# Performance work log

Hardware: AMD Instinct MI355X
Metric: run time of the kernel (lower is better)

The kernel has to match this reference:

```python
import jax, jax.numpy as jnp
import numpy as np
from jax import lax

IN_CH = 32
OUT_CH = 32
K = 7
PAD = 3
STRIDE = 1


def setup_inputs() -> dict:
    key = jax.random.key(0)
    k1, k2, k3 = jax.random.split(key, 3)
    B, T = 4, 4096
    x = jax.random.normal(k1, (B, IN_CH, T), dtype=jnp.float32)
    # weight-generating conv params: [out*in*k, in, k]
    fan_in = IN_CH * K
    W = jax.random.normal(k2, (OUT_CH * IN_CH * K, IN_CH, K), dtype=jnp.float32) / np.sqrt(fan_in).astype(np.float32)
    b = jax.random.normal(k3, (OUT_CH * IN_CH * K,), dtype=jnp.float32) * 0.01
    return {"x": x, "W": W, "b": b}


def _unfold1d(x):
    # x: [B, C, L]; pad then stack K shifted views -> [B, C, K, T]
    xp = jnp.pad(x, ((0, 0), (0, 0), (PAD, PAD)))
    Lp = xp.shape[-1]
    T = Lp - K + 1
    return jnp.stack([xp[:, :, i:i + T:STRIDE] for i in range(K)], axis=2)


def reference(x, W, b):
    B, C, L = x.shape
    # dynamic weight generation: conv1d, same padding -> [B, out*in*K, T]
    dw = lax.conv_general_dilated(
        x, W, window_strides=(STRIDE,), padding=[(PAD, PAD)],
        dimension_numbers=("NCH", "OIH", "NCH"))
    dw = dw + b[None, :, None]
    dw = dw.reshape(B, OUT_CH, IN_CH, K, -1)  # [B, O, I, K, T]
    dw = jax.nn.softmax(dw / np.sqrt(K).astype(np.float32), axis=3)
    x_unf = _unfold1d(x)  # [B, I, K, T]
    y = jnp.einsum("bckt,bockt->bot", x_unf, dw)
    return y
```

## Files before the change

kernel.cpp:

```cpp
#include <hip/hip_runtime.h>
#include <hip/hip_bf16.h>


typedef unsigned short u16;
typedef unsigned int u32;
typedef __attribute__((ext_vector_type(8))) short short8;
typedef __attribute__((ext_vector_type(4))) float f32x4;

#define IN_CH 32
#define OUT_CH 32
#define KW 7
#define TSZ 4096
#define BSZ 4
#define CONTR 224
#define NROWS 7168
#define BLK_T 512
#define XS_STRIDE 40
#define XS_ROWS (BLK_T + 6)
#define SLICE_U16 3584
#define CH_U16 25088
#define CEXP2 0.54528747f

__device__ __forceinline__ u32 f2bf(float v) {
    u32 b = __float_as_uint(v);
    return (b + 0x7fffu + ((b >> 16) & 1u)) >> 16;
}

__device__ __forceinline__ void glds16(const u16* g, u16* l) {
    __builtin_amdgcn_global_load_lds((__attribute__((address_space(1))) void*)g,
                                     (__attribute__((address_space(3))) void*)l,
                                     16, 0, 0);
}

__global__ __launch_bounds__(512)
void wprep(const float* __restrict__ W, const float* __restrict__ bias,
           u16* __restrict__ Wp, float* __restrict__ bp) {
    __shared__ float ws[CH_U16];
    int ch  = blockIdx.x;
    int tid = threadIdx.x;
    const float* src = W + (size_t)ch * CH_U16;
    #pragma unroll
    for (int it = 0; it < 49; ++it)
        ws[it * 512 + tid] = src[it * 512 + tid];
    __syncthreads();
    u16* dst = Wp + (size_t)ch * CH_U16;
    #pragma unroll
    for (int it = 0; it < 49; ++it) {
        int oidx = it * 512 + tid;
        int e  = oidx & 7;
        int pp = (oidx >> 3) & 3;
        int t1 = oidx >> 5;
        int rp = t1 % 112;
        int j  = t1 / 112;
        int p  = pp ^ ((rp >> 1) & 3);
        int c  = p * 8 + e;
        int k  = rp >> 4;
        int q  = rp & 15;
        dst[oidx] = (u16)f2bf(ws[(q * 7 + k) * CONTR + c * 7 + j]);
    }
    if (tid < 112) {
        int k = tid >> 4, q = tid & 15;
        int gp = ch * 16 + q;
        int o = gp >> 5, i = gp & 31;
        bp[ch * 112 + tid] = bias[(o * IN_CH + i) * KW + k];
    }
}

__global__ __launch_bounds__(256)
void xprep(const float* __restrict__ x, u16* __restrict__ xT) {
    int bid = blockIdx.x;
    int b = bid >> 6;
    int t0 = (bid & 63) * 64;
    __shared__ float lds[32][65];
    int tid = threadIdx.x;
    #pragma unroll
    for (int it = 0; it < 8; ++it) {
        int gi = it * 256 + tid;
        int c = gi >> 6;
        int t = gi & 63;
        lds[c][t] = x[((size_t)b * IN_CH + c) * TSZ + t0 + t];
    }
    __syncthreads();
    #pragma unroll
    for (int it = 0; it < 4; ++it) {
        int wi = it * 256 + tid;
        int t  = wi >> 4;
        int cp = wi & 15;
        u32 b0 = f2bf(lds[cp * 2][t]);
        u32 b1 = f2bf(lds[cp * 2 + 1][t]);
        ((u32*)xT)[((size_t)b * TSZ + t0 + t) * 16 + cp] = b0 | (b1 << 16);
    }
}

__global__ __launch_bounds__(512, 1)
void dconv_main(const u16* __restrict__ Wp, const float* __restrict__ bp,
                const u16* __restrict__ xT, float* __restrict__ out) {
    __shared__ u16 xs[XS_ROWS * XS_STRIDE];
    __shared__ u16 wbuf[2][CH_U16];

    int tid  = threadIdx.x;
    int lane = tid & 63;
    int wave = tid >> 6;
    int g    = lane >> 4;
    int col  = lane & 15;

    int bid = blockIdx.x;
    int b   = bid & 3;
    int tt  = (bid >> 2) & 7;
    int os  = bid >> 5;
    int t0  = tt * BLK_T;

    #pragma unroll
    for (int it = 0; it < 17; ++it) {
        int wi = it * 512 + tid;
        if (wi < XS_ROWS * 16) {
            int row = wi >> 4;
            int cp  = wi & 15;
            int t = t0 - 3 + row;
            u32 v = 0;
            if (t >= 0 && t < TSZ)
                v = ((const u32*)xT)[((size_t)b * TSZ + t) * 16 + cp];
            *(u32*)&xs[row * XS_STRIDE + cp * 2] = v;
        }
    }

    if (wave < 7) {
        const u16* src = Wp + (size_t)(os * 8) * CH_U16 + wave * SLICE_U16 + lane * 8;
        u16* dst = &wbuf[0][wave * SLICE_U16];
        #pragma unroll
        for (int it = 0; it < 7; ++it) glds16(src + it * 512, dst + it * 512);
    }
    __syncthreads();

    int laneA = col * 32 + ((g ^ ((col >> 1) & 3)) * 8);
    int colw0 = wave * 64 + col;

    float yacc[4] = {0.f, 0.f, 0.f, 0.f};

    #pragma unroll 1
    for (int ci = 0; ci < 8; ++ci) {
        int cur = ci & 1;
        if (ci < 7 && wave < 7) {
            const u16* src = Wp + (size_t)(os * 8 + ci + 1) * CH_U16 + wave * SLICE_U16 + lane * 8;
            u16* dst = &wbuf[cur ^ 1][wave * SLICE_U16];
            #pragma unroll
            for (int it = 0; it < 7; ++it) glds16(src + it * 512, dst + it * 512);
        }

        int ch = os * 8 + ci;
        int cc = ci & 1;

        f32x4 acc[7][4];
        const float* bsrc = bp + ch * 112 + g * 4;
        #pragma unroll
        for (int m = 0; m < 7; ++m) {
            f32x4 bv = *(const f32x4*)(bsrc + m * 16);
            acc[m][0] = bv; acc[m][1] = bv; acc[m][2] = bv; acc[m][3] = bv;
        }

        const u16* wl = &wbuf[cur][laneA];
        #pragma unroll
        for (int j = 0; j < 7; ++j) {
            short8 bf[4];
            #pragma unroll
            for (int ct = 0; ct < 4; ++ct)
                bf[ct] = *(const short8*)&xs[(colw0 + ct * 16 + j) * XS_STRIDE + g * 8];
            #pragma unroll
            for (int m = 0; m < 7; ++m) {
                short8 af = *(const short8*)(wl + j * SLICE_U16 + m * 512);
                acc[m][0] = __builtin_amdgcn_mfma_f32_16x16x32_bf16(af, bf[0], acc[m][0], 0, 0, 0);
                acc[m][1] = __builtin_amdgcn_mfma_f32_16x16x32_bf16(af, bf[1], acc[m][1], 0, 0, 0);
                acc[m][2] = __builtin_amdgcn_mfma_f32_16x16x32_bf16(af, bf[2], acc[m][2], 0, 0, 0);
                acc[m][3] = __builtin_amdgcn_mfma_f32_16x16x32_bf16(af, bf[3], acc[m][3], 0, 0, 0);
            }
        }

        __syncthreads();

        int ibase = cc * 16 + g * 4;
        #pragma unroll
        for (int ct = 0; ct < 4; ++ct) {
            int colw = colw0 + ct * 16;
            u32 xv0[7], xv1[7];
            #pragma unroll
            for (int k = 0; k < 7; ++k) {
                const u32* px = (const u32*)&xs[(colw + k) * XS_STRIDE + ibase];
                xv0[k] = px[0]; xv1[k] = px[1];
            }
            #pragma unroll
            for (int r = 0; r < 4; ++r) {
                float ssum = 0.f, psum = 0.f;
                #pragma unroll
                for (int k = 0; k < 7; ++k) {
                    float e = __builtin_amdgcn_exp2f(acc[k][ct][r] * CEXP2);
                    u32 w = (r & 2) ? xv1[k] : xv0[k];
                    float xf = __uint_as_float((r & 1) ? (w & 0xffff0000u) : (w << 16));
                    ssum += e;
                    psum = fmaf(e, xf, psum);
                }
                yacc[ct] += psum * __builtin_amdgcn_rcpf(ssum);
            }
        }

        if (cc == 1) {
            int o = os * 4 + (ci >> 1);
            #pragma unroll
            for (int ct = 0; ct < 4; ++ct) {
                float v = yacc[ct];
                v += __shfl_xor(v, 16, 64);
                v += __shfl_xor(v, 32, 64);
                if (lane < 16)
                    out[((size_t)b * OUT_CH + o) * TSZ + t0 + wave * 64 + ct * 16 + col] = v;
                yacc[ct] = 0.f;
            }
        }
    }
}

extern "C" void kernel_launch(void* const* d_in, const int* in_sizes, int n_in,
                              void* d_out, int out_size, void* d_ws, size_t ws_size,
                              hipStream_t stream) {
    const float* x    = (const float*)d_in[0];
    const float* W    = (const float*)d_in[1];
    const float* bias = (const float*)d_in[2];
    float* out = (float*)d_out;

    u16*   Wp = (u16*)d_ws;
    float* bp = (float*)((char*)d_ws + 3211264);
    u16*   xT = (u16*)((char*)d_ws + 3211264 + 28672);

    hipLaunchKernelGGL(wprep, dim3(64), dim3(512), 0, stream, W, bias, Wp, bp);
    hipLaunchKernelGGL(xprep, dim3(BSZ * (TSZ / 64)), dim3(256), 0, stream, x, xT);
    hipLaunchKernelGGL(dconv_main, dim3(256), dim3(512), 0, stream, Wp, bp, xT, out);
}
```

Before: 124.4 us.

## Halve time tile, single weight buffer split-half prefetch, fold softmax scale into weights

```diff
diff --git a/kernel.cpp b/kernel.cpp
--- a/kernel.cpp
+++ b/kernel.cpp
@@ -14,11 +14,14 @@
 #define BSZ 4
 #define CONTR 224
 #define NROWS 7168
-#define BLK_T 512
-#define XS_STRIDE 40
+#define BLK_T 256
+#define XS_STRIDE 42
 #define XS_ROWS (BLK_T + 6)
 #define SLICE_U16 3584
 #define CH_U16 25088
+#define HALF0_U16 14336
+#define HALF0_UNITS 28
+#define HALF1_UNITS 21
 #define CEXP2 0.54528747f
 
 __device__ __forceinline__ u32 f2bf(float v) {
@@ -56,13 +59,13 @@
         int c  = p * 8 + e;
         int k  = rp >> 4;
         int q  = rp & 15;
-        dst[oidx] = (u16)f2bf(ws[(q * 7 + k) * CONTR + c * 7 + j]);
+        dst[oidx] = (u16)f2bf(ws[(q * 7 + k) * CONTR + c * 7 + j] * CEXP2);
     }
     if (tid < 112) {
         int k = tid >> 4, q = tid & 15;
         int gp = ch * 16 + q;
         int o = gp >> 5, i = gp & 31;
-        bp[ch * 112 + tid] = bias[(o * IN_CH + i) * KW + k];
+        bp[ch * 112 + tid] = bias[(o * IN_CH + i) * KW + k] * CEXP2;
     }
 }
 
@@ -92,11 +95,11 @@
     }
 }
 
-__global__ __launch_bounds__(512, 1)
+__global__ __launch_bounds__(256, 2)
 void dconv_main(const u16* __restrict__ Wp, const float* __restrict__ bp,
                 const u16* __restrict__ xT, float* __restrict__ out) {
     __shared__ u16 xs[XS_ROWS * XS_STRIDE];
-    __shared__ u16 wbuf[2][CH_U16];
+    __shared__ u16 wbuf[CH_U16];
 
     int tid  = threadIdx.x;
     int lane = tid & 63;
@@ -106,13 +109,13 @@
 
     int bid = blockIdx.x;
     int b   = bid & 3;
-    int tt  = (bid >> 2) & 7;
-    int os  = bid >> 5;
+    int tt  = (bid >> 2) & 15;
+    int os  = bid >> 6;
     int t0  = tt * BLK_T;
 
     #pragma unroll
     for (int it = 0; it < 17; ++it) {
-        int wi = it * 512 + tid;
+        int wi = it * 256 + tid;
         if (wi < XS_ROWS * 16) {
             int row = wi >> 4;
             int cp  = wi & 15;
@@ -124,11 +127,10 @@
         }
     }
 
-    if (wave < 7) {
-        const u16* src = Wp + (size_t)(os * 8) * CH_U16 + wave * SLICE_U16 + lane * 8;
-        u16* dst = &wbuf[0][wave * SLICE_U16];
-        #pragma unroll
-        for (int it = 0; it < 7; ++it) glds16(src + it * 512, dst + it * 512);
+    {
+        const u16* src = Wp + (size_t)(os * 8) * CH_U16 + lane * 8;
+        for (int u = wave; u < HALF0_UNITS; u += 4)
+            glds16(src + u * 512, &wbuf[u * 512]);
     }
     __syncthreads();
 
@@ -139,16 +141,14 @@
 
     #pragma unroll 1
     for (int ci = 0; ci < 8; ++ci) {
-        int cur = ci & 1;
-        if (ci < 7 && wave < 7) {
-            const u16* src = Wp + (size_t)(os * 8 + ci + 1) * CH_U16 + wave * SLICE_U16 + lane * 8;
-            u16* dst = &wbuf[cur ^ 1][wave * SLICE_U16];
-            #pragma unroll
-            for (int it = 0; it < 7; ++it) glds16(src + it * 512, dst + it * 512);
-        }
-
         int ch = os * 8 + ci;
         int cc = ci & 1;
+
+        {
+            const u16* src = Wp + (size_t)ch * CH_U16 + 4 * SLICE_U16 + lane * 8;
+            for (int u = wave; u < HALF1_UNITS; u += 4)
+                glds16(src + u * 512, &wbuf[HALF0_U16 + u * 512]);
+        }
 
         f32x4 acc[7][4];
         const float* bsrc = bp + ch * 112 + g * 4;
@@ -158,24 +158,55 @@
             acc[m][0] = bv; acc[m][1] = bv; acc[m][2] = bv; acc[m][3] = bv;
         }
 
-        const u16* wl = &wbuf[cur][laneA];
-        #pragma unroll
-        for (int j = 0; j < 7; ++j) {
-            short8 bf[4];
-            #pragma unroll
-            for (int ct = 0; ct < 4; ++ct)
-                bf[ct] = *(const short8*)&xs[(colw0 + ct * 16 + j) * XS_STRIDE + g * 8];
-            #pragma unroll
-            for (int m = 0; m < 7; ++m) {
-                short8 af = *(const short8*)(wl + j * SLICE_U16 + m * 512);
-                acc[m][0] = __builtin_amdgcn_mfma_f32_16x16x32_bf16(af, bf[0], acc[m][0], 0, 0, 0);
-                acc[m][1] = __builtin_amdgcn_mfma_f32_16x16x32_bf16(af, bf[1], acc[m][1], 0, 0, 0);
-                acc[m][2] = __builtin_amdgcn_mfma_f32_16x16x32_bf16(af, bf[2], acc[m][2], 0, 0, 0);
-                acc[m][3] = __builtin_amdgcn_mfma_f32_16x16x32_bf16(af, bf[3], acc[m][3], 0, 0, 0);
-            }
-        }
-
+        __builtin_amdgcn_s_setprio(1);
+        {
+            const u16* wl = &wbuf[laneA];
+            #pragma unroll
+            for (int j = 0; j < 4; ++j) {
+                short8 bf[4];
+                #pragma unroll
+                for (int ct = 0; ct < 4; ++ct)
+                    bf[ct] = *(const short8*)&xs[(colw0 + ct * 16 + j) * XS_STRIDE + g * 8];
+                #pragma unroll
+                for (int m = 0; m < 7; ++m) {
+                    short8 af = *(const short8*)(wl + j * SLICE_U16 + m * 512);
+                    acc[m][0] = __builtin_amdgcn_mfma_f32_16x16x32_bf16(af, bf[0], acc[m][0], 0, 0, 0);
+                    acc[m][1] = __builtin_amdgcn_mfma_f32_16x16x32_bf16(af, bf[1], acc[m][1], 0, 0, 0);
+                    acc[m][2] = __builtin_amdgcn_mfma_f32_16x16x32_bf16(af, bf[2], acc[m][2], 0, 0, 0);
+                    acc[m][3] = __builtin_amdgcn_mfma_f32_16x16x32_bf16(af, bf[3], acc[m][3], 0, 0, 0);
+                }
+            }
+        }
+        __builtin_amdgcn_s_setprio(0);
         __syncthreads();
+
+        if (ci < 7) {
+            const u16* src = Wp + (size_t)(ch + 1) * CH_U16 + lane * 8;
+            for (int u = wave; u < HALF0_UNITS; u += 4)
+                glds16(src + u * 512, &wbuf[u * 512]);
+        }
+
+        __builtin_amdgcn_s_setprio(1);
+        {
+            const u16* wl = &wbuf[HALF0_U16 + laneA];
+            #pragma unroll
+            for (int jj = 0; jj < 3; ++jj) {
+                int j = 4 + jj;
+                short8 bf[4];
+                #pragma unroll
+                for (int ct = 0; ct < 4; ++ct)
+                    bf[ct] = *(const short8*)&xs[(colw0 + ct * 16 + j) * XS_STRIDE + g * 8];
+                #pragma unroll
+                for (int m = 0; m < 7; ++m) {
+                    short8 af = *(const short8*)(wl + jj * SLICE_U16 + m * 512);
+                    acc[m][0] = __builtin_amdgcn_mfma_f32_16x16x32_bf16(af, bf[0], acc[m][0], 0, 0, 0);
+                    acc[m][1] = __builtin_amdgcn_mfma_f32_16x16x32_bf16(af, bf[1], acc[m][1], 0, 0, 0);
+                    acc[m][2] = __builtin_amdgcn_mfma_f32_16x16x32_bf16(af, bf[2], acc[m][2], 0, 0, 0);
+                    acc[m][3] = __builtin_amdgcn_mfma_f32_16x16x32_bf16(af, bf[3], acc[m][3], 0, 0, 0);
+                }
+            }
+        }
+        __builtin_amdgcn_s_setprio(0);
 
         int ibase = cc * 16 + g * 4;
         #pragma unroll
@@ -192,7 +223,7 @@
                 float ssum = 0.f, psum = 0.f;
                 #pragma unroll
                 for (int k = 0; k < 7; ++k) {
-                    float e = __builtin_amdgcn_exp2f(acc[k][ct][r] * CEXP2);
+                    float e = __builtin_amdgcn_exp2f(acc[k][ct][r]);
                     u32 w = (r & 2) ? xv1[k] : xv0[k];
                     float xf = __uint_as_float((r & 1) ? (w & 0xffff0000u) : (w << 16));
                     ssum += e;
@@ -214,6 +245,7 @@
                 yacc[ct] = 0.f;
             }
         }
+        __syncthreads();
     }
 }
 
@@ -231,5 +263,5 @@
 
     hipLaunchKernelGGL(wprep, dim3(64), dim3(512), 0, stream, W, bias, Wp, bp);
     hipLaunchKernelGGL(xprep, dim3(BSZ * (TSZ / 64)), dim3(256), 0, stream, x, xT);
-    hipLaunchKernelGGL(dconv_main, dim3(256), dim3(512), 0, stream, Wp, bp, xT, out);
-}
+    hipLaunchKernelGGL(dconv_main, dim3(512), dim3(256), 0, stream, Wp, bp, xT, out);
+}
```

Measured after the change: 123.7 us. Within noise of the previous version (-0.5%).
